# Kernel tuning notes

Hardware: AMD Instinct MI355X
Metric: run time of the kernel (lower is better)

Reference implementation:

```python
import jax, jax.numpy as jnp
import numpy as np

N, H, DE, E = 100000, 64, 16, 1600000
COORD_SCALE = 0.1


def _lin_params(key, din, dout):
    kw, kb = jax.random.split(key)
    W = jax.random.normal(kw, (din, dout), dtype=jnp.float32) * 0.02
    b = jax.random.normal(kb, (dout,), dtype=jnp.float32) * 0.02
    return W, b


def setup_inputs() -> dict:
    key = jax.random.key(0)
    ks = jax.random.split(key, 10)
    h = jax.random.normal(ks[0], (N, H), dtype=jnp.float32)
    pos = jax.random.normal(ks[1], (N, 3), dtype=jnp.float32)
    edge_index = jax.random.randint(ks[2], (2, E), 0, N, dtype=jnp.int32)
    edge_attr = jax.random.normal(ks[3], (E, DE), dtype=jnp.float32)
    W_e1, b_e1 = _lin_params(ks[4], 2 * H + 1 + DE, H)
    W_e2, b_e2 = _lin_params(ks[5], H, H)
    W_c1, b_c1 = _lin_params(ks[6], H, H)
    W_c2, b_c2 = _lin_params(ks[7], H, 1)
    W_n, b_n = _lin_params(ks[8], 2 * H, H)
    ln_g = jnp.ones((H,), dtype=jnp.float32)
    ln_b = jnp.zeros((H,), dtype=jnp.float32)
    return dict(h=h, pos=pos, edge_index=edge_index, edge_attr=edge_attr,
                W_e1=W_e1, b_e1=b_e1, W_e2=W_e2, b_e2=b_e2,
                W_c1=W_c1, b_c1=b_c1, W_c2=W_c2, b_c2=b_c2,
                W_n=W_n, b_n=b_n, ln_g=ln_g, ln_b=ln_b)


def reference(h, pos, edge_index, edge_attr,
              W_e1, b_e1, W_e2, b_e2,
              W_c1, b_c1, W_c2, b_c2,
              W_n, b_n, ln_g, ln_b):
    src, dst = edge_index[0], edge_index[1]
    pos_src = pos[src]            # [E,3] gather
    pos_dst = pos[dst]
    diff = pos_dst - pos_src      # [E,3]
    dist2 = jnp.clip(jnp.sum(diff * diff, axis=-1, keepdims=True), 0.0, 1000.0)  # [E,1]
    direction = diff / jnp.sqrt(dist2 + 1e-8)

    # edge MLP: phi_e(h_i, h_j, d2, e_ij)
    edge_input = jnp.concatenate([h[src], h[dst], dist2, edge_attr], axis=-1)  # [E, 2H+1+De]
    m = jax.nn.relu(edge_input @ W_e1 + b_e1)
    m_ij = jax.nn.relu(m @ W_e2 + b_e2)  # [E,H]

    # coord MLP -> scalar coef, tanh * scale
    c = jax.nn.relu(m_ij @ W_c1 + b_c1)
    coord_coef = jnp.tanh(c @ W_c2 + b_c2) * COORD_SCALE  # [E,1]
    trans = direction * coord_coef  # [E,3]

    # scatter-add to dst
    delta_pos = jnp.zeros_like(pos).at[dst].add(trans)
    pos_out = pos + delta_pos

    agg_msg = jnp.zeros_like(h).at[dst].add(m_ij)  # [N,H]

    # node MLP + residual + LayerNorm
    h_update = jax.nn.relu(jnp.concatenate([h, agg_msg], axis=-1) @ W_n + b_n)
    x = h + h_update
    mu = jnp.mean(x, axis=-1, keepdims=True)
    var = jnp.mean((x - mu) ** 2, axis=-1, keepdims=True)
    h_out = (x - mu) / jnp.sqrt(var + 1e-5) * ln_g + ln_b
    return h_out, pos_out
```

## Files before the change

kernel.cpp:

```cpp
#include <hip/hip_runtime.h>

using f32x4  = __attribute__((ext_vector_type(4))) float;
using short8 = __attribute__((ext_vector_type(8))) short;

__device__ inline short f2bf(float x) {
    union { float f; unsigned u; } v; v.f = x;
    unsigned r = v.u + 0x7fffu + ((v.u >> 16) & 1u);
    return (short)(r >> 16);
}

__device__ inline short8 pack8(float4 a, float4 b) {
    short8 r;
    r[0] = f2bf(a.x); r[1] = f2bf(a.y); r[2] = f2bf(a.z); r[3] = f2bf(a.w);
    r[4] = f2bf(b.x); r[5] = f2bf(b.y); r[6] = f2bf(b.z); r[7] = f2bf(b.w);
    return r;
}

__device__ inline void atomic_pk_add_bf16(short* addr, unsigned pk) {
    asm volatile("global_atomic_pk_add_bf16 %0, %1, off"
                 :: "v"(addr), "v"(pk) : "memory");
}

__global__ __launch_bounds__(256) void convert_weights(
    const float* __restrict__ We1, const float* __restrict__ We2,
    const float* __restrict__ Wc1, const float* __restrict__ Wn,
    short* __restrict__ W1T, short* __restrict__ W2T,
    short* __restrict__ Wc1T, short* __restrict__ WnT)
{
    const int i = blockIdx.x * 256 + threadIdx.x;
    if (i < 64 * 160) {
        const int n = i / 160, k = i % 160;
        float v = 0.0f;
        if (k < 128)       v = We1[k * 64 + n];
        else if (k < 144)  v = We1[(129 + k - 128) * 64 + n];
        else if (k == 144) v = We1[128 * 64 + n];
        W1T[i] = f2bf(v);
    }
    if (i < 64 * 128) {
        const int n = i / 128, k = i % 128;
        WnT[i] = f2bf(Wn[k * 64 + n]);
    }
    if (i < 64 * 64) {
        const int n = i / 64, k = i % 64;
        W2T[i]  = f2bf(We2[k * 64 + n]);
        Wc1T[i] = f2bf(Wc1[k * 64 + n]);
    }
}

__global__ __launch_bounds__(256) void convert_h(
    const float* __restrict__ h, short* __restrict__ hb, int n8)
{
    const int i = blockIdx.x * 256 + threadIdx.x;
    if (i < n8) {
        const float4* h4 = reinterpret_cast<const float4*>(h);
        reinterpret_cast<short8*>(hb)[i] = pack8(h4[2 * i], h4[2 * i + 1]);
    }
}

__global__ __launch_bounds__(256, 6) void egnn_edge_mfma(
    const short* __restrict__ hb, const float* __restrict__ pos,
    const int* __restrict__ ei, const float* __restrict__ ea,
    const short* __restrict__ W1T, const short* __restrict__ W2T,
    const short* __restrict__ Wc1T,
    const float* __restrict__ be1, const float* __restrict__ be2,
    const float* __restrict__ bc1, const float* __restrict__ bc2,
    const float* __restrict__ Wc2,
    short* __restrict__ aggb, float* __restrict__ dpos, int E)
{
    __shared__ short M[4][16][72];
    __shared__ float sdir[4][3][16];
    __shared__ int   sdst[4][16];

    const int tid  = threadIdx.x;
    const int lane = tid & 63;
    const int wave = tid >> 6;
    const int r16  = lane & 15;
    const int kg   = lane >> 4;
    const int eb   = blockIdx.x * 64;

    const int e  = eb + wave * 16 + r16;
    const int ec = min(e, E - 1);
    const int src = ei[ec];
    const int dst = ei[E + ec];

    const float dx = pos[3 * dst + 0] - pos[3 * src + 0];
    const float dy = pos[3 * dst + 1] - pos[3 * src + 1];
    const float dz = pos[3 * dst + 2] - pos[3 * src + 2];
    const float d2 = fminf(dx * dx + dy * dy + dz * dz, 1000.0f);
    const float inv = 1.0f / sqrtf(d2 + 1e-8f);
    if (kg == 0) {
        sdir[wave][0][r16] = dx * inv;
        sdir[wave][1][r16] = dy * inv;
        sdir[wave][2][r16] = dz * inv;
        sdst[wave][r16] = dst;
    }

    const short8* hs = reinterpret_cast<const short8*>(hb + (size_t)src * 64);
    const short8* hd = reinterpret_cast<const short8*>(hb + (size_t)dst * 64);
    const short8 a0 = hs[kg];
    const short8 a1 = hs[4 + kg];
    const short8 a2 = hd[kg];
    const short8 a3 = hd[4 + kg];
    short8 a4 = {0, 0, 0, 0, 0, 0, 0, 0};
    if (kg < 2) {
        const float4* eap = reinterpret_cast<const float4*>(ea + (size_t)ec * 16 + kg * 8);
        a4 = pack8(eap[0], eap[1]);
    } else if (kg == 2) {
        a4[0] = f2bf(d2);
    }

    f32x4 acc1[4];
    #pragma unroll
    for (int nt = 0; nt < 4; ++nt) {
        const float b = be1[r16 + nt * 16];
        acc1[nt] = {b, b, b, b};
    }
    #pragma unroll
    for (int nt = 0; nt < 4; ++nt) {
        const short* wr = W1T + (r16 + nt * 16) * 160 + kg * 8;
        acc1[nt] = __builtin_amdgcn_mfma_f32_16x16x32_bf16(
            a0, *reinterpret_cast<const short8*>(wr), acc1[nt], 0, 0, 0);
        acc1[nt] = __builtin_amdgcn_mfma_f32_16x16x32_bf16(
            a1, *reinterpret_cast<const short8*>(wr + 32), acc1[nt], 0, 0, 0);
        acc1[nt] = __builtin_amdgcn_mfma_f32_16x16x32_bf16(
            a2, *reinterpret_cast<const short8*>(wr + 64), acc1[nt], 0, 0, 0);
        acc1[nt] = __builtin_amdgcn_mfma_f32_16x16x32_bf16(
            a3, *reinterpret_cast<const short8*>(wr + 96), acc1[nt], 0, 0, 0);
        acc1[nt] = __builtin_amdgcn_mfma_f32_16x16x32_bf16(
            a4, *reinterpret_cast<const short8*>(wr + 128), acc1[nt], 0, 0, 0);
    }
    #pragma unroll
    for (int nt = 0; nt < 4; ++nt)
        #pragma unroll
        for (int rg = 0; rg < 4; ++rg)
            M[wave][kg * 4 + rg][r16 + nt * 16] = f2bf(fmaxf(acc1[nt][rg], 0.0f));

    const short8 a5 = *reinterpret_cast<const short8*>(&M[wave][r16][kg * 8]);
    const short8 a6 = *reinterpret_cast<const short8*>(&M[wave][r16][32 + kg * 8]);
    f32x4 acc2[4];
    #pragma unroll
    for (int nt = 0; nt < 4; ++nt) {
        const float b = be2[r16 + nt * 16];
        acc2[nt] = {b, b, b, b};
    }
    #pragma unroll
    for (int nt = 0; nt < 4; ++nt) {
        const short* wr = W2T + (r16 + nt * 16) * 64 + kg * 8;
        acc2[nt] = __builtin_amdgcn_mfma_f32_16x16x32_bf16(
            a5, *reinterpret_cast<const short8*>(wr), acc2[nt], 0, 0, 0);
        acc2[nt] = __builtin_amdgcn_mfma_f32_16x16x32_bf16(
            a6, *reinterpret_cast<const short8*>(wr + 32), acc2[nt], 0, 0, 0);
    }
    #pragma unroll
    for (int nt = 0; nt < 4; ++nt)
        #pragma unroll
        for (int rg = 0; rg < 4; ++rg) {
            const float v = fmaxf(acc2[nt][rg], 0.0f);
            acc2[nt][rg] = v;
            M[wave][kg * 4 + rg][r16 + nt * 16] = f2bf(v);
        }

    const short8 a7 = *reinterpret_cast<const short8*>(&M[wave][r16][kg * 8]);
    const short8 a8 = *reinterpret_cast<const short8*>(&M[wave][r16][32 + kg * 8]);
    f32x4 acc3[4];
    #pragma unroll
    for (int nt = 0; nt < 4; ++nt) {
        const float b = bc1[r16 + nt * 16];
        acc3[nt] = {b, b, b, b};
    }
    #pragma unroll
    for (int nt = 0; nt < 4; ++nt) {
        const short* wr = Wc1T + (r16 + nt * 16) * 64 + kg * 8;
        acc3[nt] = __builtin_amdgcn_mfma_f32_16x16x32_bf16(
            a7, *reinterpret_cast<const short8*>(wr), acc3[nt], 0, 0, 0);
        acc3[nt] = __builtin_amdgcn_mfma_f32_16x16x32_bf16(
            a8, *reinterpret_cast<const short8*>(wr + 32), acc3[nt], 0, 0, 0);
    }

    float prt[4] = {0.0f, 0.0f, 0.0f, 0.0f};
    #pragma unroll
    for (int nt = 0; nt < 4; ++nt) {
        const float wv = Wc2[r16 + nt * 16];
        #pragma unroll
        for (int rg = 0; rg < 4; ++rg)
            prt[rg] += fmaxf(acc3[nt][rg], 0.0f) * wv;
    }
    #pragma unroll
    for (int off = 1; off < 16; off <<= 1)
        #pragma unroll
        for (int rg = 0; rg < 4; ++rg)
            prt[rg] += __shfl_xor(prt[rg], off);
    const float bc2v = bc2[0];

    if (r16 < 3) {
        #pragma unroll
        for (int rg = 0; rg < 4; ++rg) {
            const int erl = kg * 4 + rg;
            if (eb + wave * 16 + erl < E) {
                const float coef = tanhf(prt[rg] + bc2v) * 0.1f;
                unsafeAtomicAdd(&dpos[3 * sdst[wave][erl] + r16],
                                sdir[wave][r16][erl] * coef);
            }
        }
    }
    #pragma unroll
    for (int rg = 0; rg < 4; ++rg) {
        const int erl = kg * 4 + rg;
        if (eb + wave * 16 + erl < E) {
            short* arow = aggb + (size_t)sdst[wave][erl] * 64;
            #pragma unroll
            for (int nt = 0; nt < 4; ++nt) {
                const float v  = acc2[nt][rg];
                const float vp = __shfl_xor(v, 1);
                if ((r16 & 1) == (nt >> 1)) {
                    const int col0 = (r16 & ~1) + nt * 16;
                    const unsigned blo = (unsigned short)f2bf((r16 & 1) ? vp : v);
                    const unsigned bhi = (unsigned short)f2bf((r16 & 1) ? v : vp);
                    atomic_pk_add_bf16(arow + col0, blo | (bhi << 16));
                }
            }
        }
    }
}

__global__ __launch_bounds__(256) void egnn_node_mfma(
    const float* __restrict__ h, const short* __restrict__ hb,
    const short* __restrict__ aggb, const float* __restrict__ pos,
    const float* __restrict__ dpos, const short* __restrict__ WnT,
    const float* __restrict__ bn, const float* __restrict__ lng,
    const float* __restrict__ lnb,
    float* __restrict__ h_out, float* __restrict__ pos_out, int N)
{
    __shared__ short As[64][136];
    const int tid = threadIdx.x;
    const int n0  = blockIdx.x * 64;

    if (tid < 64) {
        const int n = n0 + tid;
        if (n < N) {
            #pragma unroll
            for (int c = 0; c < 3; ++c)
                pos_out[(size_t)3 * n + c] = pos[(size_t)3 * n + c] + dpos[(size_t)3 * n + c];
        }
    }

    {
        const int row = tid >> 2, part = tid & 3;
        const int n = n0 + row;
        if (n < N) {
            const short* sp = (part < 2) ? (hb + (size_t)n * 64 + (part & 1) * 32)
                                         : (aggb + (size_t)n * 64 + (part & 1) * 32);
            #pragma unroll
            for (int q = 0; q < 4; ++q)
                *reinterpret_cast<short8*>(&As[row][part * 32 + q * 8]) =
                    *reinterpret_cast<const short8*>(sp + q * 8);
        }
    }
    __syncthreads();

    const int lane = tid & 63;
    const int wave = tid >> 6;
    const int r16  = lane & 15;
    const int kg   = lane >> 4;
    const int mrow = wave * 16 + r16;

    f32x4 acc[4];
    #pragma unroll
    for (int nt = 0; nt < 4; ++nt) {
        const float b = bn[r16 + nt * 16];
        acc[nt] = {b, b, b, b};
    }
    #pragma unroll
    for (int kt = 0; kt < 4; ++kt) {
        short8 a = *reinterpret_cast<const short8*>(&As[mrow][kt * 32 + kg * 8]);
        #pragma unroll
        for (int nt = 0; nt < 4; ++nt) {
            short8 b = *reinterpret_cast<const short8*>(
                &WnT[(r16 + nt * 16) * 128 + kt * 32 + kg * 8]);
            acc[nt] = __builtin_amdgcn_mfma_f32_16x16x32_bf16(a, b, acc[nt], 0, 0, 0);
        }
    }

    float xv[4][4];
    #pragma unroll
    for (int rg = 0; rg < 4; ++rg) {
        const int n = n0 + wave * 16 + kg * 4 + rg;
        const bool ok = n < N;
        #pragma unroll
        for (int nt = 0; nt < 4; ++nt)
            xv[nt][rg] = (ok ? h[(size_t)n * 64 + r16 + nt * 16] : 0.0f)
                         + fmaxf(acc[nt][rg], 0.0f);
    }

    float g[4], bb[4];
    #pragma unroll
    for (int nt = 0; nt < 4; ++nt) { g[nt] = lng[r16 + nt * 16]; bb[nt] = lnb[r16 + nt * 16]; }

    #pragma unroll
    for (int rg = 0; rg < 4; ++rg) {
        float s = xv[0][rg] + xv[1][rg] + xv[2][rg] + xv[3][rg];
        #pragma unroll
        for (int off = 1; off < 16; off <<= 1) s += __shfl_xor(s, off);
        const float mu = s * 0.015625f;
        float q = 0.0f;
        #pragma unroll
        for (int nt = 0; nt < 4; ++nt) { const float d = xv[nt][rg] - mu; q += d * d; }
        #pragma unroll
        for (int off = 1; off < 16; off <<= 1) q += __shfl_xor(q, off);
        const float inv = rsqrtf(q * 0.015625f + 1e-5f);
        const int n = n0 + wave * 16 + kg * 4 + rg;
        if (n < N) {
            #pragma unroll
            for (int nt = 0; nt < 4; ++nt)
                h_out[(size_t)n * 64 + r16 + nt * 16] =
                    (xv[nt][rg] - mu) * inv * g[nt] + bb[nt];
        }
    }
}

extern "C" void kernel_launch(void* const* d_in, const int* in_sizes, int n_in,
                              void* d_out, int out_size, void* d_ws, size_t ws_size,
                              hipStream_t stream)
{
    const float* h   = (const float*)d_in[0];
    const float* pos = (const float*)d_in[1];
    const int*   ei  = (const int*)d_in[2];
    const float* ea  = (const float*)d_in[3];
    const float* We1 = (const float*)d_in[4];
    const float* be1 = (const float*)d_in[5];
    const float* We2 = (const float*)d_in[6];
    const float* be2 = (const float*)d_in[7];
    const float* Wc1 = (const float*)d_in[8];
    const float* bc1 = (const float*)d_in[9];
    const float* Wc2 = (const float*)d_in[10];
    const float* bc2 = (const float*)d_in[11];
    const float* Wn  = (const float*)d_in[12];
    const float* bn  = (const float*)d_in[13];
    const float* lng = (const float*)d_in[14];
    const float* lnb = (const float*)d_in[15];

    const int N = in_sizes[0] / 64;
    const int E = in_sizes[2] / 2;

    short* aggb = (short*)d_ws;
    float* dpos = (float*)(aggb + (size_t)N * 64);
    short* W1T  = (short*)(dpos + (size_t)N * 3);
    short* W2T  = W1T + 64 * 160;
    short* Wc1T = W2T + 64 * 64;
    short* WnT  = Wc1T + 64 * 64;
    short* hbuf = WnT + 64 * 128;

    hipMemsetAsync(d_ws, 0, (size_t)N * 140, stream);
    convert_weights<<<40, 256, 0, stream>>>(We1, We2, Wc1, Wn, W1T, W2T, Wc1T, WnT);
    convert_h<<<(N * 64 / 8 + 255) / 256, 256, 0, stream>>>(h, hbuf, N * 64 / 8);

    float* h_out   = (float*)d_out;
    float* pos_out = h_out + (size_t)N * 64;

    egnn_edge_mfma<<<(E + 63) / 64, 256, 0, stream>>>(
        hbuf, pos, ei, ea, W1T, W2T, Wc1T, be1, be2, bc1, bc2, Wc2, aggb, dpos, E);
    egnn_node_mfma<<<(N + 63) / 64, 256, 0, stream>>>(
        h, hbuf, aggb, pos, dpos, WnT, bn, lng, lnb, h_out, pos_out, N);
}
```

Measured before the change: 614.5 us.

## Replace atomic scatter with CSR-by-destination gather in edge kernel

Builds a destination-sorted edge list each call with count, single-block scan and fill kernels. The edge kernel then assigns one wave per destination node and processes its incoming edges in chunks of 16. Messages and coordinate updates are summed in fp32 registers and written once per node, replacing bf16 packed atomics and float atomics. Costs include three extra passes over the edge indices, a serial one-block scan, padding waste when node degree is not a multiple of 16, and load imbalance across waves.

```diff
diff --git a/kernel.cpp b/kernel.cpp
--- a/kernel.cpp
+++ b/kernel.cpp
@@ -14,11 +14,6 @@
     r[0] = f2bf(a.x); r[1] = f2bf(a.y); r[2] = f2bf(a.z); r[3] = f2bf(a.w);
     r[4] = f2bf(b.x); r[5] = f2bf(b.y); r[6] = f2bf(b.z); r[7] = f2bf(b.w);
     return r;
-}
-
-__device__ inline void atomic_pk_add_bf16(short* addr, unsigned pk) {
-    asm volatile("global_atomic_pk_add_bf16 %0, %1, off"
-                 :: "v"(addr), "v"(pk) : "memory");
 }
 
 __global__ __launch_bounds__(256) void convert_weights(
@@ -57,7 +52,49 @@
     }
 }
 
-__global__ __launch_bounds__(256, 6) void egnn_edge_mfma(
+__global__ __launch_bounds__(256) void count_kernel(
+    const int* __restrict__ ei, int* __restrict__ cnt, int E)
+{
+    const int e = blockIdx.x * 256 + threadIdx.x;
+    if (e < E) atomicAdd(&cnt[ei[E + e]], 1);
+}
+
+__global__ __launch_bounds__(1024) void scan_kernel(
+    const int* __restrict__ cnt, int* __restrict__ start, int N)
+{
+    __shared__ int part[1024];
+    const int tid = threadIdx.x;
+    const int per = (N + 1023) >> 10;
+    const int lo = tid * per;
+    const int hi = min(lo + per, N);
+    int s = 0;
+    for (int i = lo; i < hi; ++i) s += cnt[i];
+    part[tid] = s;
+    __syncthreads();
+    for (int off = 1; off < 1024; off <<= 1) {
+        int v = (tid >= off) ? part[tid - off] : 0;
+        __syncthreads();
+        part[tid] += v;
+        __syncthreads();
+    }
+    int off0 = (tid == 0) ? 0 : part[tid - 1];
+    for (int i = lo; i < hi; ++i) { start[i] = off0; off0 += cnt[i]; }
+    if (tid == 1023) start[N] = part[1023];
+}
+
+__global__ __launch_bounds__(256) void fill_kernel(
+    const int* __restrict__ ei, const int* __restrict__ start,
+    int* __restrict__ cursor, int* __restrict__ eidbuf, int E)
+{
+    const int e = blockIdx.x * 256 + threadIdx.x;
+    if (e < E) {
+        const int d = ei[E + e];
+        const int slot = start[d] + atomicAdd(&cursor[d], 1);
+        eidbuf[slot] = e;
+    }
+}
+
+__global__ __launch_bounds__(256) void egnn_edge_gather(
     const short* __restrict__ hb, const float* __restrict__ pos,
     const int* __restrict__ ei, const float* __restrict__ ea,
     const short* __restrict__ W1T, const short* __restrict__ W2T,
@@ -65,162 +102,175 @@
     const float* __restrict__ be1, const float* __restrict__ be2,
     const float* __restrict__ bc1, const float* __restrict__ bc2,
     const float* __restrict__ Wc2,
-    short* __restrict__ aggb, float* __restrict__ dpos, int E)
+    const int* __restrict__ start, const int* __restrict__ eidbuf,
+    short* __restrict__ aggb, float* __restrict__ dpos, int N, int E)
 {
     __shared__ short M[4][16][72];
     __shared__ float sdir[4][3][16];
-    __shared__ int   sdst[4][16];
 
     const int tid  = threadIdx.x;
     const int lane = tid & 63;
     const int wave = tid >> 6;
     const int r16  = lane & 15;
     const int kg   = lane >> 4;
-    const int eb   = blockIdx.x * 64;
-
-    const int e  = eb + wave * 16 + r16;
-    const int ec = min(e, E - 1);
-    const int src = ei[ec];
-    const int dst = ei[E + ec];
-
-    const float dx = pos[3 * dst + 0] - pos[3 * src + 0];
-    const float dy = pos[3 * dst + 1] - pos[3 * src + 1];
-    const float dz = pos[3 * dst + 2] - pos[3 * src + 2];
-    const float d2 = fminf(dx * dx + dy * dy + dz * dz, 1000.0f);
-    const float inv = 1.0f / sqrtf(d2 + 1e-8f);
-    if (kg == 0) {
-        sdir[wave][0][r16] = dx * inv;
-        sdir[wave][1][r16] = dy * inv;
-        sdir[wave][2][r16] = dz * inv;
-        sdst[wave][r16] = dst;
-    }
-
-    const short8* hs = reinterpret_cast<const short8*>(hb + (size_t)src * 64);
-    const short8* hd = reinterpret_cast<const short8*>(hb + (size_t)dst * 64);
-    const short8 a0 = hs[kg];
-    const short8 a1 = hs[4 + kg];
-    const short8 a2 = hd[kg];
-    const short8 a3 = hd[4 + kg];
-    short8 a4 = {0, 0, 0, 0, 0, 0, 0, 0};
-    if (kg < 2) {
-        const float4* eap = reinterpret_cast<const float4*>(ea + (size_t)ec * 16 + kg * 8);
-        a4 = pack8(eap[0], eap[1]);
-    } else if (kg == 2) {
-        a4[0] = f2bf(d2);
-    }
-
-    f32x4 acc1[4];
+    const int n    = blockIdx.x * 4 + wave;
+    if (n >= N) return;
+
+    const int s0 = start[n];
+    const int s1 = start[n + 1];
+
+    const short8* hd = reinterpret_cast<const short8*>(hb + (size_t)n * 64);
+    const short8 hd0 = hd[kg];
+    const short8 hd1 = hd[4 + kg];
+    const float pdx = pos[3 * n + 0], pdy = pos[3 * n + 1], pdz = pos[3 * n + 2];
+
+    float b1v[4], b2v[4], b3v[4], w2v[4];
     #pragma unroll
     for (int nt = 0; nt < 4; ++nt) {
-        const float b = be1[r16 + nt * 16];
-        acc1[nt] = {b, b, b, b};
-    }
-    #pragma unroll
-    for (int nt = 0; nt < 4; ++nt) {
-        const short* wr = W1T + (r16 + nt * 16) * 160 + kg * 8;
-        acc1[nt] = __builtin_amdgcn_mfma_f32_16x16x32_bf16(
-            a0, *reinterpret_cast<const short8*>(wr), acc1[nt], 0, 0, 0);
-        acc1[nt] = __builtin_amdgcn_mfma_f32_16x16x32_bf16(
-            a1, *reinterpret_cast<const short8*>(wr + 32), acc1[nt], 0, 0, 0);
-        acc1[nt] = __builtin_amdgcn_mfma_f32_16x16x32_bf16(
-            a2, *reinterpret_cast<const short8*>(wr + 64), acc1[nt], 0, 0, 0);
-        acc1[nt] = __builtin_amdgcn_mfma_f32_16x16x32_bf16(
-            a3, *reinterpret_cast<const short8*>(wr + 96), acc1[nt], 0, 0, 0);
-        acc1[nt] = __builtin_amdgcn_mfma_f32_16x16x32_bf16(
-            a4, *reinterpret_cast<const short8*>(wr + 128), acc1[nt], 0, 0, 0);
-    }
-    #pragma unroll
-    for (int nt = 0; nt < 4; ++nt)
-        #pragma unroll
-        for (int rg = 0; rg < 4; ++rg)
-            M[wave][kg * 4 + rg][r16 + nt * 16] = f2bf(fmaxf(acc1[nt][rg], 0.0f));
-
-    const short8 a5 = *reinterpret_cast<const short8*>(&M[wave][r16][kg * 8]);
-    const short8 a6 = *reinterpret_cast<const short8*>(&M[wave][r16][32 + kg * 8]);
-    f32x4 acc2[4];
-    #pragma unroll
-    for (int nt = 0; nt < 4; ++nt) {
-        const float b = be2[r16 + nt * 16];
-        acc2[nt] = {b, b, b, b};
-    }
-    #pragma unroll
-    for (int nt = 0; nt < 4; ++nt) {
-        const short* wr = W2T + (r16 + nt * 16) * 64 + kg * 8;
-        acc2[nt] = __builtin_amdgcn_mfma_f32_16x16x32_bf16(
-            a5, *reinterpret_cast<const short8*>(wr), acc2[nt], 0, 0, 0);
-        acc2[nt] = __builtin_amdgcn_mfma_f32_16x16x32_bf16(
-            a6, *reinterpret_cast<const short8*>(wr + 32), acc2[nt], 0, 0, 0);
-    }
-    #pragma unroll
-    for (int nt = 0; nt < 4; ++nt)
+        b1v[nt] = be1[r16 + nt * 16];
+        b2v[nt] = be2[r16 + nt * 16];
+        b3v[nt] = bc1[r16 + nt * 16];
+        w2v[nt] = Wc2[r16 + nt * 16];
+    }
+    const float bc2v = bc2[0];
+
+    float cs0 = 0.0f, cs1 = 0.0f, cs2 = 0.0f, cs3 = 0.0f;
+    float t0 = 0.0f, t1 = 0.0f, t2 = 0.0f;
+
+    for (int c0 = s0; c0 < s1; c0 += 16) {
+        const int slot = min(c0 + r16, s1 - 1);
+        const int eid  = eidbuf[slot];
+        const int src  = ei[eid];
+
+        const float dx = pdx - pos[3 * src + 0];
+        const float dy = pdy - pos[3 * src + 1];
+        const float dz = pdz - pos[3 * src + 2];
+        const float d2 = fminf(dx * dx + dy * dy + dz * dz, 1000.0f);
+        const float inv = 1.0f / sqrtf(d2 + 1e-8f);
+        if (kg == 0) {
+            sdir[wave][0][r16] = dx * inv;
+            sdir[wave][1][r16] = dy * inv;
+            sdir[wave][2][r16] = dz * inv;
+        }
+
+        const short8* hs = reinterpret_cast<const short8*>(hb + (size_t)src * 64);
+        const short8 a0 = hs[kg];
+        const short8 a1 = hs[4 + kg];
+        short8 a4 = {0, 0, 0, 0, 0, 0, 0, 0};
+        if (kg < 2) {
+            const float4* eap = reinterpret_cast<const float4*>(
+                ea + (size_t)eid * 16 + kg * 8);
+            a4 = pack8(eap[0], eap[1]);
+        } else if (kg == 2) {
+            a4[0] = f2bf(d2);
+        }
+
+        f32x4 acc1[4];
+        #pragma unroll
+        for (int nt = 0; nt < 4; ++nt)
+            acc1[nt] = {b1v[nt], b1v[nt], b1v[nt], b1v[nt]};
+        #pragma unroll
+        for (int nt = 0; nt < 4; ++nt) {
+            const short* wr = W1T + (r16 + nt * 16) * 160 + kg * 8;
+            acc1[nt] = __builtin_amdgcn_mfma_f32_16x16x32_bf16(
+                a0, *reinterpret_cast<const short8*>(wr), acc1[nt], 0, 0, 0);
+            acc1[nt] = __builtin_amdgcn_mfma_f32_16x16x32_bf16(
+                a1, *reinterpret_cast<const short8*>(wr + 32), acc1[nt], 0, 0, 0);
+            acc1[nt] = __builtin_amdgcn_mfma_f32_16x16x32_bf16(
+                hd0, *reinterpret_cast<const short8*>(wr + 64), acc1[nt], 0, 0, 0);
+            acc1[nt] = __builtin_amdgcn_mfma_f32_16x16x32_bf16(
+                hd1, *reinterpret_cast<const short8*>(wr + 96), acc1[nt], 0, 0, 0);
+            acc1[nt] = __builtin_amdgcn_mfma_f32_16x16x32_bf16(
+                a4, *reinterpret_cast<const short8*>(wr + 128), acc1[nt], 0, 0, 0);
+        }
+        #pragma unroll
+        for (int nt = 0; nt < 4; ++nt)
+            #pragma unroll
+            for (int rg = 0; rg < 4; ++rg)
+                M[wave][kg * 4 + rg][r16 + nt * 16] = f2bf(fmaxf(acc1[nt][rg], 0.0f));
+
+        const short8 a5 = *reinterpret_cast<const short8*>(&M[wave][r16][kg * 8]);
+        const short8 a6 = *reinterpret_cast<const short8*>(&M[wave][r16][32 + kg * 8]);
+        f32x4 acc2[4];
+        #pragma unroll
+        for (int nt = 0; nt < 4; ++nt)
+            acc2[nt] = {b2v[nt], b2v[nt], b2v[nt], b2v[nt]};
+        #pragma unroll
+        for (int nt = 0; nt < 4; ++nt) {
+            const short* wr = W2T + (r16 + nt * 16) * 64 + kg * 8;
+            acc2[nt] = __builtin_amdgcn_mfma_f32_16x16x32_bf16(
+                a5, *reinterpret_cast<const short8*>(wr), acc2[nt], 0, 0, 0);
+            acc2[nt] = __builtin_amdgcn_mfma_f32_16x16x32_bf16(
+                a6, *reinterpret_cast<const short8*>(wr + 32), acc2[nt], 0, 0, 0);
+        }
+        #pragma unroll
+        for (int nt = 0; nt < 4; ++nt)
+            #pragma unroll
+            for (int rg = 0; rg < 4; ++rg) {
+                const float v = fmaxf(acc2[nt][rg], 0.0f);
+                acc2[nt][rg] = v;
+                M[wave][kg * 4 + rg][r16 + nt * 16] = f2bf(v);
+            }
+
         #pragma unroll
         for (int rg = 0; rg < 4; ++rg) {
-            const float v = fmaxf(acc2[nt][rg], 0.0f);
-            acc2[nt][rg] = v;
-            M[wave][kg * 4 + rg][r16 + nt * 16] = f2bf(v);
-        }
-
-    const short8 a7 = *reinterpret_cast<const short8*>(&M[wave][r16][kg * 8]);
-    const short8 a8 = *reinterpret_cast<const short8*>(&M[wave][r16][32 + kg * 8]);
-    f32x4 acc3[4];
-    #pragma unroll
-    for (int nt = 0; nt < 4; ++nt) {
-        const float b = bc1[r16 + nt * 16];
-        acc3[nt] = {b, b, b, b};
-    }
-    #pragma unroll
-    for (int nt = 0; nt < 4; ++nt) {
-        const short* wr = Wc1T + (r16 + nt * 16) * 64 + kg * 8;
-        acc3[nt] = __builtin_amdgcn_mfma_f32_16x16x32_bf16(
-            a7, *reinterpret_cast<const short8*>(wr), acc3[nt], 0, 0, 0);
-        acc3[nt] = __builtin_amdgcn_mfma_f32_16x16x32_bf16(
-            a8, *reinterpret_cast<const short8*>(wr + 32), acc3[nt], 0, 0, 0);
-    }
-
-    float prt[4] = {0.0f, 0.0f, 0.0f, 0.0f};
-    #pragma unroll
-    for (int nt = 0; nt < 4; ++nt) {
-        const float wv = Wc2[r16 + nt * 16];
-        #pragma unroll
-        for (int rg = 0; rg < 4; ++rg)
-            prt[rg] += fmaxf(acc3[nt][rg], 0.0f) * wv;
-    }
-    #pragma unroll
-    for (int off = 1; off < 16; off <<= 1)
-        #pragma unroll
-        for (int rg = 0; rg < 4; ++rg)
-            prt[rg] += __shfl_xor(prt[rg], off);
-    const float bc2v = bc2[0];
-
-    if (r16 < 3) {
+            if (c0 + kg * 4 + rg < s1) {
+                cs0 += acc2[0][rg]; cs1 += acc2[1][rg];
+                cs2 += acc2[2][rg]; cs3 += acc2[3][rg];
+            }
+        }
+
+        const short8 a7 = *reinterpret_cast<const short8*>(&M[wave][r16][kg * 8]);
+        const short8 a8 = *reinterpret_cast<const short8*>(&M[wave][r16][32 + kg * 8]);
+        f32x4 acc3[4];
+        #pragma unroll
+        for (int nt = 0; nt < 4; ++nt)
+            acc3[nt] = {b3v[nt], b3v[nt], b3v[nt], b3v[nt]};
+        #pragma unroll
+        for (int nt = 0; nt < 4; ++nt) {
+            const short* wr = Wc1T + (r16 + nt * 16) * 64 + kg * 8;
+            acc3[nt] = __builtin_amdgcn_mfma_f32_16x16x32_bf16(
+                a7, *reinterpret_cast<const short8*>(wr), acc3[nt], 0, 0, 0);
+            acc3[nt] = __builtin_amdgcn_mfma_f32_16x16x32_bf16(
+                a8, *reinterpret_cast<const short8*>(wr + 32), acc3[nt], 0, 0, 0);
+        }
+
+        float prt[4] = {0.0f, 0.0f, 0.0f, 0.0f};
+        #pragma unroll
+        for (int nt = 0; nt < 4; ++nt)
+            #pragma unroll
+            for (int rg = 0; rg < 4; ++rg)
+                prt[rg] += fmaxf(acc3[nt][rg], 0.0f) * w2v[nt];
+        #pragma unroll
+        for (int off = 1; off < 16; off <<= 1)
+            #pragma unroll
+            for (int rg = 0; rg < 4; ++rg)
+                prt[rg] += __shfl_xor(prt[rg], off);
+
         #pragma unroll
         for (int rg = 0; rg < 4; ++rg) {
-            const int erl = kg * 4 + rg;
-            if (eb + wave * 16 + erl < E) {
-                const float coef = tanhf(prt[rg] + bc2v) * 0.1f;
-                unsafeAtomicAdd(&dpos[3 * sdst[wave][erl] + r16],
-                                sdir[wave][r16][erl] * coef);
+            const int row = kg * 4 + rg;
+            if (c0 + row < s1) {
+                const float cf = tanhf(prt[rg] + bc2v) * 0.1f;
+                t0 += sdir[wave][0][row] * cf;
+                t1 += sdir[wave][1][row] * cf;
+                t2 += sdir[wave][2][row] * cf;
             }
         }
     }
-    #pragma unroll
-    for (int rg = 0; rg < 4; ++rg) {
-        const int erl = kg * 4 + rg;
-        if (eb + wave * 16 + erl < E) {
-            short* arow = aggb + (size_t)sdst[wave][erl] * 64;
-            #pragma unroll
-            for (int nt = 0; nt < 4; ++nt) {
-                const float v  = acc2[nt][rg];
-                const float vp = __shfl_xor(v, 1);
-                if ((r16 & 1) == (nt >> 1)) {
-                    const int col0 = (r16 & ~1) + nt * 16;
-                    const unsigned blo = (unsigned short)f2bf((r16 & 1) ? vp : v);
-                    const unsigned bhi = (unsigned short)f2bf((r16 & 1) ? v : vp);
-                    atomic_pk_add_bf16(arow + col0, blo | (bhi << 16));
-                }
-            }
-        }
-    }
+
+    #pragma unroll
+    for (int off = 16; off <= 32; off <<= 1) {
+        cs0 += __shfl_xor(cs0, off); cs1 += __shfl_xor(cs1, off);
+        cs2 += __shfl_xor(cs2, off); cs3 += __shfl_xor(cs3, off);
+        t0  += __shfl_xor(t0,  off); t1  += __shfl_xor(t1,  off);
+        t2  += __shfl_xor(t2,  off);
+    }
+
+    const float myv = (kg == 0) ? cs0 : (kg == 1) ? cs1 : (kg == 2) ? cs2 : cs3;
+    aggb[(size_t)n * 64 + kg * 16 + r16] = f2bf(myv);
+    if (lane < 3)
+        dpos[3 * n + lane] = (lane == 0) ? t0 : (lane == 1) ? t1 : t2;
 }
 
 __global__ __launch_bounds__(256) void egnn_node_mfma(
@@ -342,23 +392,31 @@
     const int N = in_sizes[0] / 64;
     const int E = in_sizes[2] / 2;
 
-    short* aggb = (short*)d_ws;
-    float* dpos = (float*)(aggb + (size_t)N * 64);
-    short* W1T  = (short*)(dpos + (size_t)N * 3);
-    short* W2T  = W1T + 64 * 160;
-    short* Wc1T = W2T + 64 * 64;
-    short* WnT  = Wc1T + 64 * 64;
-    short* hbuf = WnT + 64 * 128;
-
-    hipMemsetAsync(d_ws, 0, (size_t)N * 140, stream);
+    short* aggb  = (short*)d_ws;
+    short* hbuf  = aggb + (size_t)N * 64;
+    short* W1T   = hbuf + (size_t)N * 64;
+    short* W2T   = W1T + 64 * 160;
+    short* Wc1T  = W2T + 64 * 64;
+    short* WnT   = Wc1T + 64 * 64;
+    float* dpos  = (float*)(WnT + 64 * 128);
+    int*   startp = (int*)(dpos + (size_t)N * 3);
+    int*   cnt    = startp + (N + 1);
+    int*   cursor = cnt + N;
+    int*   eidbuf = cursor + N;
+
+    hipMemsetAsync(cnt, 0, (size_t)2 * N * sizeof(int), stream);
     convert_weights<<<40, 256, 0, stream>>>(We1, We2, Wc1, Wn, W1T, W2T, Wc1T, WnT);
     convert_h<<<(N * 64 / 8 + 255) / 256, 256, 0, stream>>>(h, hbuf, N * 64 / 8);
+    count_kernel<<<(E + 255) / 256, 256, 0, stream>>>(ei, cnt, E);
+    scan_kernel<<<1, 1024, 0, stream>>>(cnt, startp, N);
+    fill_kernel<<<(E + 255) / 256, 256, 0, stream>>>(ei, startp, cursor, eidbuf, E);
 
     float* h_out   = (float*)d_out;
     float* pos_out = h_out + (size_t)N * 64;
 
-    egnn_edge_mfma<<<(E + 63) / 64, 256, 0, stream>>>(
-        hbuf, pos, ei, ea, W1T, W2T, Wc1T, be1, be2, bc1, bc2, Wc2, aggb, dpos, E);
+    egnn_edge_gather<<<(N + 3) / 4, 256, 0, stream>>>(
+        hbuf, pos, ei, ea, W1T, W2T, Wc1T, be1, be2, bc1, bc2, Wc2,
+        startp, eidbuf, aggb, dpos, N, E);
     egnn_node_mfma<<<(N + 63) / 64, 256, 0, stream>>>(
         h, hbuf, aggb, pos, dpos, WnT, bn, lng, lnb, h_out, pos_out, N);
 }
```

Result: slower. 1.309 ms (+113.0%).

## Sort edges by destination and pre-reduce runs before atomic scatter

Applied to the files above, without the earlier changes.

Adds a counting sort of edges by destination (count, single-block scan, fill kernels) and has the edge kernel process edges in sorted order. Within each 16-edge group, consecutive edges sharing a destination are summed with wave shuffles and issued as one set of atomics, which cuts the atomic traffic to aggb and dpos. In exchange it adds three extra launches plus a serial 1024-thread scan. The edge kernel now gathers edge attributes and indices through an indirection, giving scattered reads of ea. Random destinations make runs short, so few atomics may actually be saved.

```diff
diff --git a/kernel.cpp b/kernel.cpp
--- a/kernel.cpp
+++ b/kernel.cpp
@@ -57,43 +57,80 @@
     }
 }
 
-__global__ __launch_bounds__(256, 6) void egnn_edge_mfma(
+__global__ __launch_bounds__(256) void count_kernel(
+    const int* __restrict__ ei, int* __restrict__ cnt, int E)
+{
+    const int e = blockIdx.x * 256 + threadIdx.x;
+    if (e < E) atomicAdd(&cnt[ei[E + e]], 1);
+}
+
+__global__ __launch_bounds__(1024) void scan_kernel(
+    const int* __restrict__ cnt, int* __restrict__ start, int N)
+{
+    __shared__ int part[1024];
+    const int tid = threadIdx.x;
+    const int per = (N + 1023) >> 10;
+    const int lo = tid * per;
+    const int hi = min(lo + per, N);
+    int s = 0;
+    for (int i = lo; i < hi; ++i) s += cnt[i];
+    part[tid] = s;
+    __syncthreads();
+    for (int off = 1; off < 1024; off <<= 1) {
+        int v = (tid >= off) ? part[tid - off] : 0;
+        __syncthreads();
+        part[tid] += v;
+        __syncthreads();
+    }
+    int off0 = (tid == 0) ? 0 : part[tid - 1];
+    for (int i = lo; i < hi; ++i) { start[i] = off0; off0 += cnt[i]; }
+    if (tid == 1023) start[N] = part[1023];
+}
+
+__global__ __launch_bounds__(256) void fill_kernel(
+    const int* __restrict__ ei, const int* __restrict__ start,
+    int* __restrict__ cursor, int* __restrict__ eidbuf, int E)
+{
+    const int e = blockIdx.x * 256 + threadIdx.x;
+    if (e < E) {
+        const int d = ei[E + e];
+        const int slot = start[d] + atomicAdd(&cursor[d], 1);
+        eidbuf[slot] = e;
+    }
+}
+
+__global__ __launch_bounds__(256, 6) void egnn_edge_sorted(
     const short* __restrict__ hb, const float* __restrict__ pos,
     const int* __restrict__ ei, const float* __restrict__ ea,
     const short* __restrict__ W1T, const short* __restrict__ W2T,
     const short* __restrict__ Wc1T,
     const float* __restrict__ be1, const float* __restrict__ be2,
     const float* __restrict__ bc1, const float* __restrict__ bc2,
-    const float* __restrict__ Wc2,
+    const float* __restrict__ Wc2, const int* __restrict__ eidbuf,
     short* __restrict__ aggb, float* __restrict__ dpos, int E)
 {
     __shared__ short M[4][16][72];
-    __shared__ float sdir[4][3][16];
-    __shared__ int   sdst[4][16];
 
     const int tid  = threadIdx.x;
     const int lane = tid & 63;
     const int wave = tid >> 6;
     const int r16  = lane & 15;
     const int kg   = lane >> 4;
-    const int eb   = blockIdx.x * 64;
-
-    const int e  = eb + wave * 16 + r16;
-    const int ec = min(e, E - 1);
-    const int src = ei[ec];
-    const int dst = ei[E + ec];
-
-    const float dx = pos[3 * dst + 0] - pos[3 * src + 0];
-    const float dy = pos[3 * dst + 1] - pos[3 * src + 1];
-    const float dz = pos[3 * dst + 2] - pos[3 * src + 2];
+
+    const int slot  = blockIdx.x * 64 + wave * 16 + r16;
+    const bool vrow = slot < E;
+    const int slotc = min(slot, E - 1);
+    const int eid   = eidbuf[slotc];
+    const int src   = ei[eid];
+    const int dst   = ei[E + eid];
+    const int dkey  = vrow ? dst : -1;
+
+    float dx = pos[3 * dst + 0] - pos[3 * src + 0];
+    float dy = pos[3 * dst + 1] - pos[3 * src + 1];
+    float dz = pos[3 * dst + 2] - pos[3 * src + 2];
     const float d2 = fminf(dx * dx + dy * dy + dz * dz, 1000.0f);
     const float inv = 1.0f / sqrtf(d2 + 1e-8f);
-    if (kg == 0) {
-        sdir[wave][0][r16] = dx * inv;
-        sdir[wave][1][r16] = dy * inv;
-        sdir[wave][2][r16] = dz * inv;
-        sdst[wave][r16] = dst;
-    }
+    dx *= inv; dy *= inv; dz *= inv;
 
     const short8* hs = reinterpret_cast<const short8*>(hb + (size_t)src * 64);
     const short8* hd = reinterpret_cast<const short8*>(hb + (size_t)dst * 64);
@@ -103,7 +140,7 @@
     const short8 a3 = hd[4 + kg];
     short8 a4 = {0, 0, 0, 0, 0, 0, 0, 0};
     if (kg < 2) {
-        const float4* eap = reinterpret_cast<const float4*>(ea + (size_t)ec * 16 + kg * 8);
+        const float4* eap = reinterpret_cast<const float4*>(ea + (size_t)eid * 16 + kg * 8);
         a4 = pack8(eap[0], eap[1]);
     } else if (kg == 2) {
         a4[0] = f2bf(d2);
@@ -177,49 +214,83 @@
             a8, *reinterpret_cast<const short8*>(wr + 32), acc3[nt], 0, 0, 0);
     }
 
-    float prt[4] = {0.0f, 0.0f, 0.0f, 0.0f};
+    float cf[4] = {0.0f, 0.0f, 0.0f, 0.0f};
     #pragma unroll
     for (int nt = 0; nt < 4; ++nt) {
         const float wv = Wc2[r16 + nt * 16];
         #pragma unroll
         for (int rg = 0; rg < 4; ++rg)
-            prt[rg] += fmaxf(acc3[nt][rg], 0.0f) * wv;
+            cf[rg] += fmaxf(acc3[nt][rg], 0.0f) * wv;
     }
     #pragma unroll
     for (int off = 1; off < 16; off <<= 1)
         #pragma unroll
         for (int rg = 0; rg < 4; ++rg)
-            prt[rg] += __shfl_xor(prt[rg], off);
+            cf[rg] += __shfl_xor(cf[rg], off);
     const float bc2v = bc2[0];
-
-    if (r16 < 3) {
+    #pragma unroll
+    for (int rg = 0; rg < 4; ++rg)
+        cf[rg] = tanhf(cf[rg] + bc2v) * 0.1f;
+
+    const int srcl = ((r16 >> 2) << 4) + r16;
+    const float c0 = __shfl(cf[0], srcl);
+    const float c1 = __shfl(cf[1], srcl);
+    const float c2 = __shfl(cf[2], srcl);
+    const float c3 = __shfl(cf[3], srcl);
+    const int rsel = r16 & 3;
+    const float cfown = (rsel == 0) ? c0 : (rsel == 1) ? c1 : (rsel == 2) ? c2 : c3;
+
+    int rstart = 0;
+    while (rstart < 16) {
+        const int dcur = __shfl(dkey, rstart);
+        const bool inrun = (dkey == dcur) && (r16 >= rstart);
+        const unsigned long long bm = __ballot(inrun);
+        const int len = __popc((unsigned)bm & 0xFFFFu);
+        const int rend = rstart + len;
+
+        float s0 = 0.0f, s1 = 0.0f, s2 = 0.0f, s3 = 0.0f;
         #pragma unroll
         for (int rg = 0; rg < 4; ++rg) {
-            const int erl = kg * 4 + rg;
-            if (eb + wave * 16 + erl < E) {
-                const float coef = tanhf(prt[rg] + bc2v) * 0.1f;
-                unsafeAtomicAdd(&dpos[3 * sdst[wave][erl] + r16],
-                                sdir[wave][r16][erl] * coef);
+            const int row = (kg << 2) + rg;
+            if (row >= rstart && row < rend) {
+                s0 += acc2[0][rg]; s1 += acc2[1][rg];
+                s2 += acc2[2][rg]; s3 += acc2[3][rg];
             }
         }
-    }
-    #pragma unroll
-    for (int rg = 0; rg < 4; ++rg) {
-        const int erl = kg * 4 + rg;
-        if (eb + wave * 16 + erl < E) {
-            short* arow = aggb + (size_t)sdst[wave][erl] * 64;
+        s0 += __shfl_xor(s0, 16); s0 += __shfl_xor(s0, 32);
+        s1 += __shfl_xor(s1, 16); s1 += __shfl_xor(s1, 32);
+        s2 += __shfl_xor(s2, 16); s2 += __shfl_xor(s2, 32);
+        s3 += __shfl_xor(s3, 16); s3 += __shfl_xor(s3, 32);
+
+        float tx = inrun ? cfown * dx : 0.0f;
+        float ty = inrun ? cfown * dy : 0.0f;
+        float tz = inrun ? cfown * dz : 0.0f;
+        #pragma unroll
+        for (int off = 1; off < 16; off <<= 1) {
+            tx += __shfl_xor(tx, off);
+            ty += __shfl_xor(ty, off);
+            tz += __shfl_xor(tz, off);
+        }
+
+        if (dcur >= 0) {
             #pragma unroll
             for (int nt = 0; nt < 4; ++nt) {
-                const float v  = acc2[nt][rg];
+                const float v  = (nt == 0) ? s0 : (nt == 1) ? s1 : (nt == 2) ? s2 : s3;
                 const float vp = __shfl_xor(v, 1);
-                if ((r16 & 1) == (nt >> 1)) {
+                if (kg == 0 && ((r16 & 1) == (nt >> 1))) {
                     const int col0 = (r16 & ~1) + nt * 16;
                     const unsigned blo = (unsigned short)f2bf((r16 & 1) ? vp : v);
                     const unsigned bhi = (unsigned short)f2bf((r16 & 1) ? v : vp);
-                    atomic_pk_add_bf16(arow + col0, blo | (bhi << 16));
+                    atomic_pk_add_bf16(aggb + (size_t)dcur * 64 + col0,
+                                       blo | (bhi << 16));
                 }
             }
-        }
+            if (kg == 0 && r16 < 3) {
+                const float tv = (r16 == 0) ? tx : (r16 == 1) ? ty : tz;
+                unsafeAtomicAdd(&dpos[3 * dcur + r16], tv);
+            }
+        }
+        rstart = rend;
     }
 }
 
@@ -342,23 +413,31 @@
     const int N = in_sizes[0] / 64;
     const int E = in_sizes[2] / 2;
 
-    short* aggb = (short*)d_ws;
-    float* dpos = (float*)(aggb + (size_t)N * 64);
-    short* W1T  = (short*)(dpos + (size_t)N * 3);
-    short* W2T  = W1T + 64 * 160;
-    short* Wc1T = W2T + 64 * 64;
-    short* WnT  = Wc1T + 64 * 64;
-    short* hbuf = WnT + 64 * 128;
-
-    hipMemsetAsync(d_ws, 0, (size_t)N * 140, stream);
+    short* aggb   = (short*)d_ws;
+    float* dpos   = (float*)(aggb + (size_t)N * 64);
+    int*   cnt    = (int*)(dpos + (size_t)3 * N);
+    int*   cursor = cnt + N;
+    int*   startp = cursor + N;
+    int*   eidbuf = startp + N + 4;
+    short* W1T    = (short*)(eidbuf + E);
+    short* W2T    = W1T + 64 * 160;
+    short* Wc1T   = W2T + 64 * 64;
+    short* WnT    = Wc1T + 64 * 64;
+    short* hbuf   = WnT + 64 * 128;
+
+    hipMemsetAsync(d_ws, 0, (size_t)N * 148, stream);
     convert_weights<<<40, 256, 0, stream>>>(We1, We2, Wc1, Wn, W1T, W2T, Wc1T, WnT);
     convert_h<<<(N * 64 / 8 + 255) / 256, 256, 0, stream>>>(h, hbuf, N * 64 / 8);
+    count_kernel<<<(E + 255) / 256, 256, 0, stream>>>(ei, cnt, E);
+    scan_kernel<<<1, 1024, 0, stream>>>(cnt, startp, N);
+    fill_kernel<<<(E + 255) / 256, 256, 0, stream>>>(ei, startp, cursor, eidbuf, E);
 
     float* h_out   = (float*)d_out;
     float* pos_out = h_out + (size_t)N * 64;
 
-    egnn_edge_mfma<<<(E + 63) / 64, 256, 0, stream>>>(
-        hbuf, pos, ei, ea, W1T, W2T, Wc1T, be1, be2, bc1, bc2, Wc2, aggb, dpos, E);
+    egnn_edge_sorted<<<(E + 63) / 64, 256, 0, stream>>>(
+        hbuf, pos, ei, ea, W1T, W2T, Wc1T, be1, be2, bc1, bc2, Wc2,
+        eidbuf, aggb, dpos, E);
     egnn_node_mfma<<<(N + 63) / 64, 256, 0, stream>>>(
         h, hbuf, aggb, pos, dpos, WnT, bn, lng, lnb, h_out, pos_out, N);
 }
```

Result: slower. 739.3 us (+20.3%).
